# Kernel optimization log

Measured on AMD Instinct MI355X. Metric: run time of the kernel, lower is better.

The kernel has to match this reference:

```python
import jax, jax.numpy as jnp
import numpy as np

L, B, D_IN, D = 96, 32, 4, 128   # leaves, batch, input feats, dim_feedforward
NB, NC = 3, 6                    # n_blocks, n_classes
E = L * (L - 1)                  # directed edges, no self-loops


def _adjacency():
    # one-hot receiver/sender matrices, shape (E, L)
    pairs = np.array([(i, j) for i in range(L) for j in range(L) if i != j])
    recv, send = pairs[:, 0], pairs[:, 1]
    rr = np.zeros((E, L), np.float32); rr[np.arange(E), recv] = 1.0
    rs = np.zeros((E, L), np.float32); rs[np.arange(E), send] = 1.0
    return rr, rs


def setup_inputs() -> dict:
    key = jax.random.key(0)
    ks = jax.random.split(key, 24)
    rr, rs = _adjacency()
    inp = {
        'inputs': jax.random.normal(ks[0], (L, B, D_IN), jnp.float32),
        'rel_rec': jnp.broadcast_to(jnp.asarray(rr), (B, E, L)),
        'rel_send': jnp.broadcast_to(jnp.asarray(rs), (B, E, L)),
    }
    s = 0.1
    # initial MLP: D_IN -> D -> D
    inp['W0a'] = s * jax.random.normal(ks[1], (D_IN, D)); inp['b0a'] = jnp.zeros((D,))
    inp['W0b'] = s * jax.random.normal(ks[2], (D, D));    inp['b0b'] = jnp.zeros((D,))
    # per-block edge MLP (2D -> D -> D) and node MLP (D -> D -> D), stacked over NB
    inp['eW1'] = s * jax.random.normal(ks[3], (NB, 2 * D, D)); inp['eb1'] = jnp.zeros((NB, D))
    inp['eW2'] = s * jax.random.normal(ks[4], (NB, D, D));     inp['eb2'] = jnp.zeros((NB, D))
    inp['nW1'] = s * jax.random.normal(ks[5], (NB, D, D));     inp['nb1'] = jnp.zeros((NB, D))
    inp['nW2'] = s * jax.random.normal(ks[6], (NB, D, D));     inp['nb2'] = jnp.zeros((NB, D))
    # final MLP: 2D -> D -> NC
    inp['fW1'] = s * jax.random.normal(ks[7], (2 * D, D)); inp['fb1'] = jnp.zeros((D,))
    inp['fW2'] = s * jax.random.normal(ks[8], (D, NC));    inp['fb2'] = jnp.zeros((NC,))
    return inp


def _mlp(x, W1, b1, W2, b2):
    return jax.nn.elu(jax.nn.elu(x @ W1 + b1) @ W2 + b2)


def reference(inputs, rel_rec, rel_send, W0a, b0a, W0b, b0b,
              eW1, eb1, eW2, eb2, nW1, nb1, nW2, nb2,
              fW1, fb1, fW2, fb2):
    def node2edge(h):
        # (b,l,d) -> (b,E,2d): cat([senders, receivers])
        senders = jnp.einsum('bel,bld->bed', rel_send, h)
        receivers = jnp.einsum('bel,bld->bed', rel_rec, h)
        return jnp.concatenate([senders, receivers], axis=2)

    def edge2node(h):
        # (b,E,d) -> (b,l,d), mean over incoming edges
        incoming = jnp.einsum('bel,bed->bld', rel_rec, h)
        denom = rel_rec.sum(1)[:, 1]  # (b,)
        return incoming / denom[:, None, None]

    x = jnp.transpose(inputs, (1, 0, 2))           # (b, l, d_in)
    x = _mlp(x, W0a, b0a, W0b, b0b)                # (b, l, D)
    x = node2edge(x)                               # (b, E, 2D)
    for i in range(NB):
        x = _mlp(x, eW1[i], eb1[i], eW2[i], eb2[i])  # (b, E, D)
        x = edge2node(x)                             # (b, l, D)
        x = _mlp(x, nW1[i], nb1[i], nW2[i], nb2[i])  # (b, l, D)
        x = node2edge(x)                             # (b, E, 2D)
    out = jax.nn.elu(x @ fW1 + fb1) @ fW2 + fb2    # (b, E, NC)
    return out
```

## Files before the change

kernel.cpp:

```cpp
#include <hip/hip_runtime.h>
#include <hip/hip_bf16.h>

#define LN 96
#define BN 32
#define DM 128
#define EPN 95

typedef __attribute__((ext_vector_type(8))) short s16x8;
typedef __attribute__((ext_vector_type(4))) float f32x4;

__device__ __forceinline__ float eluf(float x){ return x > 0.f ? x : __expf(x) - 1.f; }
__device__ __forceinline__ unsigned short f2bf(float f){
    unsigned u = __float_as_uint(f);
    return (unsigned short)((u + 0x7fff + ((u >> 16) & 1)) >> 16);
}
__device__ __forceinline__ float bf2f(unsigned short h){ return __uint_as_float(((unsigned)h) << 16); }
__device__ __forceinline__ unsigned cvtpk(float lo, float hi){
    unsigned r;
    asm("v_cvt_pk_bf16_f32 %0, %1, %2" : "=v"(r) : "v"(lo), "v"(hi));
    return r;
}

struct SrcTab { const float* p[19]; };

__global__ void conv_pack_kernel(SrcTab tab, unsigned short* __restrict__ hi,
                                 unsigned short* __restrict__ lo){
    int tid = blockIdx.x * 256 + threadIdx.x;
    int m = tid >> 11, c = tid & 2047;
    int l = c & 63, f = c >> 6;
    int n = (f >> 2) * 16 + (l & 15);
    int k0 = (f & 3) * 32 + (l >> 4) * 8;
    union { unsigned short us[8]; uint4 v; } ph, pl;
#pragma unroll
    for (int e = 0; e < 8; ++e){
        float x;
        if (m == 18) x = (n < 6) ? tab.p[18][(k0 + e) * 6 + n] : 0.f;
        else         x = tab.p[m][(k0 + e) * DM + n];
        unsigned short h = f2bf(x);
        ph.us[e] = h;
        pl.us[e] = f2bf(x - bf2f(h));
    }
    *(uint4*)(hi + (size_t)tid * 8) = ph.v;
    *(uint4*)(lo + (size_t)tid * 8) = pl.v;
}

__device__ __forceinline__ void mmw(const char* atile, int l,
                                    const unsigned short* __restrict__ whW,
                                    const unsigned short* __restrict__ wlW,
                                    f32x4 acc[2]) {
    const int l15 = l & 15, kgrp = l >> 4;
    s16x8 a[4];
#pragma unroll
    for (int ks = 0; ks < 4; ++ks)
        a[ks] = *(const s16x8*)(atile + ((l15 * 256 + (ks * 32 + kgrp * 8) * 2) ^ ((l15 & 7) << 4)));
#pragma unroll
    for (int ntl = 0; ntl < 2; ++ntl) {
#pragma unroll
        for (int ks = 0; ks < 4; ++ks) {
            s16x8 bh = *(const s16x8*)(whW + (size_t)((ntl * 4 + ks) * 64 + l) * 8);
            acc[ntl] = __builtin_amdgcn_mfma_f32_16x16x32_bf16(a[ks], bh, acc[ntl], 0, 0, 0);
        }
#pragma unroll
        for (int ks = 0; ks < 4; ++ks) {
            s16x8 bl = *(const s16x8*)(wlW + (size_t)((ntl * 4 + ks) * 64 + l) * 8);
            acc[ntl] = __builtin_amdgcn_mfma_f32_16x16x32_bf16(a[ks], bl, acc[ntl], 0, 0, 0);
        }
    }
}

__device__ __forceinline__ void store_act(char* atile, int l, int w, f32x4 acc[2]) {
    const int l15 = l & 15, kgrp = l >> 4;
#pragma unroll
    for (int ntl = 0; ntl < 2; ++ntl)
#pragma unroll
        for (int i = 0; i < 4; ++i) {
            int row = kgrp * 4 + i;
            int col = (2 * w + ntl) * 16 + l15;
            *(unsigned short*)(atile + ((row * 256 + col * 2) ^ ((row & 7) << 4))) = f2bf(eluf(acc[ntl][i]));
        }
}

__global__ __launch_bounds__(256) void node0_kernel(
    const float* __restrict__ in,
    const float* __restrict__ W0a, const float* __restrict__ b0a,
    const unsigned short* __restrict__ w2h, const unsigned short* __restrict__ w2l,
    const float* __restrict__ b2,
    const unsigned short* __restrict__ wsh, const unsigned short* __restrict__ wsl,
    const unsigned short* __restrict__ wrh, const unsigned short* __restrict__ wrl,
    const float* __restrict__ bp,
    unsigned short* __restrict__ hs, unsigned short* __restrict__ hr) {
    __shared__ char atile[16 * 256];
    const int t = threadIdx.x;
    const int q = blockIdx.x >> 5, bblk = blockIdx.x & 31;
    const int row0 = bblk * LN + q * 16;
    const int l = t & 63, w = t >> 6;
    const int l15 = l & 15, kgrp = l >> 4;

    {
        int rr = t >> 4, qq = t & 15, c0 = qq * 8;
        int swz = (rr & 7) << 4;
        union { unsigned short us[8]; uint4 v; } pk;
        int row = row0 + rr;
        int b = row / LN, ll = row - b * LN;
        float4 x = *(const float4*)(in + (size_t)(ll * BN + b) * 4);
#pragma unroll
        for (int j = 0; j < 8; ++j) {
            int cc = c0 + j;
            float a = b0a[cc] + x.x * W0a[cc] + x.y * W0a[DM + cc]
                    + x.z * W0a[2 * DM + cc] + x.w * W0a[3 * DM + cc];
            pk.us[j] = f2bf(eluf(a));
        }
        *(uint4*)(atile + ((rr * 256 + c0 * 2) ^ swz)) = pk.v;
    }
    __syncthreads();

    f32x4 acc[2];
    const int cA = (2 * w) * 16 + l15, cB = (2 * w + 1) * 16 + l15;
    {
        float ba = b2[cA], bb = b2[cB];
        acc[0] = (f32x4){ba, ba, ba, ba};
        acc[1] = (f32x4){bb, bb, bb, bb};
        mmw(atile, l, w2h + w * 4096, w2l + w * 4096, acc);
        __syncthreads();
        store_act(atile, l, w, acc);
        __syncthreads();
    }
    acc[0] = (f32x4){0.f, 0.f, 0.f, 0.f};
    acc[1] = (f32x4){0.f, 0.f, 0.f, 0.f};
    mmw(atile, l, wsh + w * 4096, wsl + w * 4096, acc);
#pragma unroll
    for (int ntl = 0; ntl < 2; ++ntl)
#pragma unroll
        for (int i = 0; i < 4; ++i)
            hs[(size_t)(row0 + kgrp * 4 + i) * DM + (2 * w + ntl) * 16 + l15] = f2bf(acc[ntl][i]);
    {
        float ba = bp[cA], bb = bp[cB];
        acc[0] = (f32x4){ba, ba, ba, ba};
        acc[1] = (f32x4){bb, bb, bb, bb};
        mmw(atile, l, wrh + w * 4096, wrl + w * 4096, acc);
    }
#pragma unroll
    for (int ntl = 0; ntl < 2; ++ntl)
#pragma unroll
        for (int i = 0; i < 4; ++i)
            hr[(size_t)(row0 + kgrp * 4 + i) * DM + (2 * w + ntl) * 16 + l15] = f2bf(acc[ntl][i]);
}

__global__ __launch_bounds__(256) void edge_node_kernel(
    const unsigned short* __restrict__ hsIn, const unsigned short* __restrict__ hrIn,
    const unsigned short* __restrict__ whi, const unsigned short* __restrict__ wlo,
    int eslot, const float* __restrict__ eb2v,
    int s1, int s2, int sS,
    const float* __restrict__ b1, const float* __restrict__ b2, const float* __restrict__ bp,
    unsigned short* __restrict__ hsOut, unsigned short* __restrict__ hrOut) {
    __shared__ char tileA[LN * 256];
    __shared__ char tileB[LN * 256];
    __shared__ float hrL[6 * DM];
    __shared__ float gL[6 * DM];
    __shared__ char actA[16 * 256];
    __shared__ char actB[16 * 256];
    const int blk = blockIdx.x;
    const int rg = blk >> 5, b = blk & 31;
    const int r0 = rg * 6;
    const int t = threadIdx.x;
    const int w = t >> 6, l = t & 63;
    const int l15 = l & 15, kgrp = l >> 4;

    if (t < 192) {
        int rr = t >> 5, c4 = (t & 31) * 4;
        ushort4 hv = *(const ushort4*)(hrIn + ((size_t)(b * LN + r0 + rr)) * DM + c4);
        float4 fv = make_float4(bf2f(hv.x), bf2f(hv.y), bf2f(hv.z), bf2f(hv.w));
        *(float4*)(hrL + rr * DM + c4) = fv;
    }
    s16x8 bfr[2][4];
#pragma unroll
    for (int ntl = 0; ntl < 2; ++ntl)
#pragma unroll
        for (int ks = 0; ks < 4; ++ks)
            bfr[ntl][ks] = *(const s16x8*)(whi + (size_t)eslot * 16384 +
                           (size_t)(((2 * w + ntl) * 4 + ks) * 64 + l) * 8);
    float b20 = eb2v[(2 * w) * 16 + l15], b21 = eb2v[(2 * w + 1) * 16 + l15];
    __syncthreads();

    const unsigned short* hsBase = hsIn + (size_t)(b * LN) * DM;
    for (int pr = 0; pr < 3; ++pr) {
        const int rA = r0 + pr * 2, rB = rA + 1;
#pragma unroll
        for (int ch = 0; ch < 6; ++ch) {
            uint4 hv[2];
            int rrs[2], c0s[2], tts[2];
#pragma unroll
            for (int k = 0; k < 2; ++k) {
                int task = t + (ch * 2 + k) * 256;
                int tt = task >= 1536;
                int rem = task - tt * 1536;
                int rr = rem >> 4, c0 = (rem & 15) * 8;
                rrs[k] = rr; c0s[k] = c0; tts[k] = tt;
                int r = tt ? rB : rA;
                int j = rr + (rr >= r);
                hv[k] = *(const uint4*)(hsBase + (size_t)j * DM + c0);
            }
#pragma unroll
            for (int k = 0; k < 2; ++k) {
                int rr = rrs[k], c0 = c0s[k], tt = tts[k];
                const unsigned short* us = (const unsigned short*)&hv[k];
                const float* rp = hrL + (pr * 2 + tt) * DM + c0;
                f32x4 v0 = *(const f32x4*)rp, v1 = *(const f32x4*)(rp + 4);
                float e0 = eluf(bf2f(us[0]) + v0[0]), e1 = eluf(bf2f(us[1]) + v0[1]);
                float e2 = eluf(bf2f(us[2]) + v0[2]), e3 = eluf(bf2f(us[3]) + v0[3]);
                float e4 = eluf(bf2f(us[4]) + v1[0]), e5 = eluf(bf2f(us[5]) + v1[1]);
                float e6 = eluf(bf2f(us[6]) + v1[2]), e7 = eluf(bf2f(us[7]) + v1[3]);
                uint4 pk;
                pk.x = cvtpk(e0, e1); pk.y = cvtpk(e2, e3);
                pk.z = cvtpk(e4, e5); pk.w = cvtpk(e6, e7);
                *(uint4*)((tt ? tileB : tileA) + ((rr * 256 + c0 * 2) ^ ((rr & 7) << 4))) = pk;
            }
        }
        __syncthreads();
#pragma unroll
        for (int slot = 0; slot < 2; ++slot) {
            const char* tile = slot ? tileB : tileA;
            f32x4 acc[6][2] = {};
#pragma unroll
            for (int mt = 0; mt < 6; ++mt) {
                int arow = mt * 16 + l15;
                const char* rb = tile + arow * 256;
                int swz = (arow & 7) << 4;
#pragma unroll
                for (int ks = 0; ks < 4; ++ks) {
                    s16x8 a = *(const s16x8*)(rb + (((ks * 32 + kgrp * 8) * 2) ^ swz));
                    acc[mt][0] = __builtin_amdgcn_mfma_f32_16x16x32_bf16(a, bfr[0][ks], acc[mt][0], 0, 0, 0);
                    acc[mt][1] = __builtin_amdgcn_mfma_f32_16x16x32_bf16(a, bfr[1][ks], acc[mt][1], 0, 0, 0);
                }
            }
            float cs0 = 0.f, cs1 = 0.f;
#pragma unroll
            for (int mt = 0; mt < 6; ++mt)
#pragma unroll
                for (int i = 0; i < 4; ++i) {
                    int row = mt * 16 + kgrp * 4 + i;
                    if (row < EPN) {
                        cs0 += eluf(acc[mt][0][i] + b20);
                        cs1 += eluf(acc[mt][1][i] + b21);
                    }
                }
            cs0 += __shfl_xor(cs0, 16); cs0 += __shfl_xor(cs0, 32);
            cs1 += __shfl_xor(cs1, 16); cs1 += __shfl_xor(cs1, 32);
            if (l < 16) {
                gL[(pr * 2 + slot) * DM + (2 * w) * 16 + l]     = cs0 * (1.f / 95.f);
                gL[(pr * 2 + slot) * DM + (2 * w + 1) * 16 + l] = cs1 * (1.f / 95.f);
            }
        }
        __syncthreads();
    }

    {
        int rr = t >> 4, q = t & 15, c0 = q * 8;
        int swz = (rr & 7) << 4;
        union { unsigned short us[8]; uint4 v; } pk;
        if (rr < 6) {
            const float* src = gL + rr * DM + c0;
            float4 f0 = *(const float4*)(src);
            float4 f1 = *(const float4*)(src + 4);
            pk.us[0] = f2bf(f0.x); pk.us[1] = f2bf(f0.y); pk.us[2] = f2bf(f0.z); pk.us[3] = f2bf(f0.w);
            pk.us[4] = f2bf(f1.x); pk.us[5] = f2bf(f1.y); pk.us[6] = f2bf(f1.z); pk.us[7] = f2bf(f1.w);
        } else pk.v = make_uint4(0, 0, 0, 0);
        *(uint4*)(actA + ((rr * 256 + c0 * 2) ^ swz)) = pk.v;
    }
    __syncthreads();

    f32x4 acc[2];
    const int cA = (2 * w) * 16 + l15, cB = (2 * w + 1) * 16 + l15;
    {
        float ba = b1[cA], bb = b1[cB];
        acc[0] = (f32x4){ba, ba, ba, ba};
        acc[1] = (f32x4){bb, bb, bb, bb};
        mmw(actA, l, whi + (size_t)s1 * 16384 + w * 4096, wlo + (size_t)s1 * 16384 + w * 4096, acc);
        __syncthreads();
        store_act(actB, l, w, acc);
        __syncthreads();
    }
    {
        float ba = b2[cA], bb = b2[cB];
        acc[0] = (f32x4){ba, ba, ba, ba};
        acc[1] = (f32x4){bb, bb, bb, bb};
        mmw(actB, l, whi + (size_t)s2 * 16384 + w * 4096, wlo + (size_t)s2 * 16384 + w * 4096, acc);
        __syncthreads();
        store_act(actA, l, w, acc);
        __syncthreads();
    }
    acc[0] = (f32x4){0.f, 0.f, 0.f, 0.f};
    acc[1] = (f32x4){0.f, 0.f, 0.f, 0.f};
    mmw(actA, l, whi + (size_t)sS * 16384 + w * 4096, wlo + (size_t)sS * 16384 + w * 4096, acc);
#pragma unroll
    for (int ntl = 0; ntl < 2; ++ntl)
#pragma unroll
        for (int i = 0; i < 4; ++i) {
            int row = kgrp * 4 + i;
            if (row < 6)
                hsOut[(size_t)(b * LN + r0 + row) * DM + (2 * w + ntl) * 16 + l15] = f2bf(acc[ntl][i]);
        }
    {
        float ba = bp[cA], bb = bp[cB];
        acc[0] = (f32x4){ba, ba, ba, ba};
        acc[1] = (f32x4){bb, bb, bb, bb};
        mmw(actA, l, whi + (size_t)(sS + 1) * 16384 + w * 4096, wlo + (size_t)(sS + 1) * 16384 + w * 4096, acc);
    }
#pragma unroll
    for (int ntl = 0; ntl < 2; ++ntl)
#pragma unroll
        for (int i = 0; i < 4; ++i) {
            int row = kgrp * 4 + i;
            if (row < 6)
                hrOut[(size_t)(b * LN + r0 + row) * DM + (2 * w + ntl) * 16 + l15] = f2bf(acc[ntl][i]);
        }
}

__global__ __launch_bounds__(256) void final_kernel(
    const unsigned short* __restrict__ hs, const unsigned short* __restrict__ hr,
    const unsigned short* __restrict__ wfh, const unsigned short* __restrict__ wfl,
    const float* __restrict__ fb2, float* __restrict__ out) {
    __shared__ char tA[LN * 256];
    __shared__ char tB[LN * 256];
    __shared__ float hrL[6 * DM];
    const int blk = blockIdx.x;
    const int rg = blk >> 5, b = blk & 31;
    const int r0 = rg * 6;
    const int t = threadIdx.x;
    const int w = t >> 6, l = t & 63;
    const int l15 = l & 15, kgrp = l >> 4;

    if (t < 192) {
        int rr = t >> 5, c4 = (t & 31) * 4;
        ushort4 hv = *(const ushort4*)(hr + ((size_t)(b * LN + r0 + rr)) * DM + c4);
        float4 fv = make_float4(bf2f(hv.x), bf2f(hv.y), bf2f(hv.z), bf2f(hv.w));
        *(float4*)(hrL + rr * DM + c4) = fv;
    }
    s16x8 fh[4], fl4[4];
#pragma unroll
    for (int ks = 0; ks < 4; ++ks) {
        fh[ks]  = *(const s16x8*)(wfh + (size_t)(ks * 64 + l) * 8);
        fl4[ks] = *(const s16x8*)(wfl + (size_t)(ks * 64 + l) * 8);
    }
    float fbv = (l15 < 6) ? fb2[l15] : 0.f;
    __syncthreads();

    const unsigned short* hsBase = hs + (size_t)(b * LN) * DM;
    for (int pr = 0; pr < 3; ++pr) {
        const int rA = r0 + pr * 2, rB = rA + 1;
#pragma unroll
        for (int ch = 0; ch < 6; ++ch) {
            uint4 hv[2];
            int rrs[2], c0s[2], tts[2];
#pragma unroll
            for (int k = 0; k < 2; ++k) {
                int task = t + (ch * 2 + k) * 256;
                int tt = task >= 1536;
                int rem = task - tt * 1536;
                int rr = rem >> 4, c0 = (rem & 15) * 8;
                rrs[k] = rr; c0s[k] = c0; tts[k] = tt;
                int r = tt ? rB : rA;
                int j = rr + (rr >= r);
                hv[k] = *(const uint4*)(hsBase + (size_t)j * DM + c0);
            }
#pragma unroll
            for (int k = 0; k < 2; ++k) {
                int rr = rrs[k], c0 = c0s[k], tt = tts[k];
                const unsigned short* us = (const unsigned short*)&hv[k];
                const float* rp = hrL + (pr * 2 + tt) * DM + c0;
                f32x4 v0 = *(const f32x4*)rp, v1 = *(const f32x4*)(rp + 4);
                float e0 = eluf(bf2f(us[0]) + v0[0]), e1 = eluf(bf2f(us[1]) + v0[1]);
                float e2 = eluf(bf2f(us[2]) + v0[2]), e3 = eluf(bf2f(us[3]) + v0[3]);
                float e4 = eluf(bf2f(us[4]) + v1[0]), e5 = eluf(bf2f(us[5]) + v1[1]);
                float e6 = eluf(bf2f(us[6]) + v1[2]), e7 = eluf(bf2f(us[7]) + v1[3]);
                uint4 pk;
                pk.x = cvtpk(e0, e1); pk.y = cvtpk(e2, e3);
                pk.z = cvtpk(e4, e5); pk.w = cvtpk(e6, e7);
                *(uint4*)((tt ? tB : tA) + ((rr * 256 + c0 * 2) ^ ((rr & 7) << 4))) = pk;
            }
        }
        __syncthreads();
        for (int q = w; q < 12; q += 4) {
            int tt = q >= 6;
            int mt = q - tt * 6;
            const char* tile = tt ? tB : tA;
            int r = tt ? rB : rA;
            int arow = mt * 16 + l15;
            const char* rb = tile + arow * 256;
            int swz = (arow & 7) << 4;
            s16x8 a[4];
#pragma unroll
            for (int ks = 0; ks < 4; ++ks)
                a[ks] = *(const s16x8*)(rb + (((ks * 32 + kgrp * 8) * 2) ^ swz));
            f32x4 acc = (f32x4){fbv, fbv, fbv, fbv};
#pragma unroll
            for (int ks = 0; ks < 4; ++ks)
                acc = __builtin_amdgcn_mfma_f32_16x16x32_bf16(a[ks], fh[ks], acc, 0, 0, 0);
#pragma unroll
            for (int ks = 0; ks < 4; ++ks)
                acc = __builtin_amdgcn_mfma_f32_16x16x32_bf16(a[ks], fl4[ks], acc, 0, 0, 0);
            if (l15 < 6) {
                float* ob = out + ((size_t)b * (LN * EPN) + (size_t)r * EPN) * 6;
#pragma unroll
                for (int i = 0; i < 4; ++i) {
                    int row = mt * 16 + kgrp * 4 + i;
                    if (row < EPN) ob[(size_t)row * 6 + l15] = acc[i];
                }
            }
        }
        __syncthreads();
    }
}

extern "C" void kernel_launch(void* const* d_in, const int* in_sizes, int n_in,
                              void* d_out, int out_size, void* d_ws, size_t ws_size,
                              hipStream_t stream) {
    const float* inputs = (const float*)d_in[0];
    const float* W0a = (const float*)d_in[3];
    const float* b0a = (const float*)d_in[4];
    const float* W0b = (const float*)d_in[5];
    const float* b0b = (const float*)d_in[6];
    const float* eW1 = (const float*)d_in[7];
    const float* eb1 = (const float*)d_in[8];
    const float* eW2 = (const float*)d_in[9];
    const float* eb2 = (const float*)d_in[10];
    const float* nW1 = (const float*)d_in[11];
    const float* nb1 = (const float*)d_in[12];
    const float* nW2 = (const float*)d_in[13];
    const float* nb2 = (const float*)d_in[14];
    const float* fW1 = (const float*)d_in[15];
    const float* fb1 = (const float*)d_in[16];
    const float* fW2 = (const float*)d_in[17];
    const float* fb2 = (const float*)d_in[18];
    float* out = (float*)d_out;

    const int NR = BN * LN;
    unsigned short* whi = (unsigned short*)d_ws;
    unsigned short* wlo = whi + 19 * 16384;
    unsigned short* hsA = wlo + 19 * 16384;
    unsigned short* hrA = hsA + (NR + 1) * DM;
    unsigned short* hsB = hrA + NR * DM;
    unsigned short* hrB = hsB + (NR + 1) * DM;

    SrcTab tab;
    tab.p[0] = eW2;          tab.p[1] = eW2 + 16384;  tab.p[2] = eW2 + 32768;
    tab.p[3] = W0b;
    tab.p[4] = eW1;          tab.p[5] = eW1 + 16384;
    tab.p[6] = nW1;          tab.p[7] = nW2;          tab.p[8] = eW1 + 32768;  tab.p[9]  = eW1 + 49152;
    tab.p[10] = nW1 + 16384; tab.p[11] = nW2 + 16384; tab.p[12] = eW1 + 65536; tab.p[13] = eW1 + 81920;
    tab.p[14] = nW1 + 32768; tab.p[15] = nW2 + 32768; tab.p[16] = fW1;         tab.p[17] = fW1 + 16384;
    tab.p[18] = fW2;

    #define WM(m) (whi + (m) * 16384), (wlo + (m) * 16384)

    conv_pack_kernel<<<152, 256, 0, stream>>>(tab, whi, wlo);
    node0_kernel<<<192, 256, 0, stream>>>(inputs, W0a, b0a, WM(3), b0b, WM(4), WM(5), eb1, hsA, hrA);
    edge_node_kernel<<<512, 256, 0, stream>>>(hsA, hrA, whi, wlo, 0, eb2,
                                              6, 7, 8, nb1, nb2, eb1 + DM, hsB, hrB);
    edge_node_kernel<<<512, 256, 0, stream>>>(hsB, hrB, whi, wlo, 1, eb2 + DM,
                                              10, 11, 12, nb1 + DM, nb2 + DM, eb1 + 2 * DM, hsA, hrA);
    edge_node_kernel<<<512, 256, 0, stream>>>(hsA, hrA, whi, wlo, 2, eb2 + 2 * DM,
                                              14, 15, 16, nb1 + 2 * DM, nb2 + 2 * DM, fb1, hsB, hrB);
    final_kernel<<<512, 256, 0, stream>>>(hsB, hrB, WM(18), fb2, out);
    #undef WM
}
```

Measured before the change: 118.3 us.

## Split edge_node work into 4-node groups and alias shared memory buffers

Each edge_node block now handles 4 receiver nodes instead of 6, raising the grid from 512 to 768 blocks so the work spreads more evenly across CUs. The shared-memory buffers are merged into one aliased region, with the small activation tiles reusing the edge tile space and hrL/gL stored as bf16, which shrinks LDS per block and may allow more resident blocks. The cost is more blocks each reloading the edge weights and repeating the small node MLP, plus slightly lower precision on the cached hr values.

Result: slower. 122.2 us (+3.4%).

```diff
diff --git a/kernel.cpp b/kernel.cpp
--- a/kernel.cpp
+++ b/kernel.cpp
@@ -153,24 +153,23 @@
     int s1, int s2, int sS,
     const float* __restrict__ b1, const float* __restrict__ b2, const float* __restrict__ bp,
     unsigned short* __restrict__ hsOut, unsigned short* __restrict__ hrOut) {
-    __shared__ char tileA[LN * 256];
-    __shared__ char tileB[LN * 256];
-    __shared__ float hrL[6 * DM];
-    __shared__ float gL[6 * DM];
-    __shared__ char actA[16 * 256];
-    __shared__ char actB[16 * 256];
+    __shared__ char smem[49152 + 1024 + 1024];
+    char* tileA = smem;
+    char* tileB = smem + 24576;
+    unsigned short* hrL = (unsigned short*)(smem + 49152);
+    unsigned short* gL  = (unsigned short*)(smem + 49152 + 1024);
+    char* actA = smem;
+    char* actB = smem + 4096;
     const int blk = blockIdx.x;
     const int rg = blk >> 5, b = blk & 31;
-    const int r0 = rg * 6;
+    const int r0 = rg * 4;
     const int t = threadIdx.x;
     const int w = t >> 6, l = t & 63;
     const int l15 = l & 15, kgrp = l >> 4;
 
-    if (t < 192) {
-        int rr = t >> 5, c4 = (t & 31) * 4;
-        ushort4 hv = *(const ushort4*)(hrIn + ((size_t)(b * LN + r0 + rr)) * DM + c4);
-        float4 fv = make_float4(bf2f(hv.x), bf2f(hv.y), bf2f(hv.z), bf2f(hv.w));
-        *(float4*)(hrL + rr * DM + c4) = fv;
+    if (t < 64) {
+        int rr = t >> 4, c8 = (t & 15) * 8;
+        *(uint4*)(hrL + rr * DM + c8) = *(const uint4*)(hrIn + ((size_t)(b * LN + r0 + rr)) * DM + c8);
     }
     s16x8 bfr[2][4];
 #pragma unroll
@@ -183,7 +182,7 @@
     __syncthreads();
 
     const unsigned short* hsBase = hsIn + (size_t)(b * LN) * DM;
-    for (int pr = 0; pr < 3; ++pr) {
+    for (int pr = 0; pr < 2; ++pr) {
         const int rA = r0 + pr * 2, rB = rA + 1;
 #pragma unroll
         for (int ch = 0; ch < 6; ++ch) {
@@ -204,12 +203,12 @@
             for (int k = 0; k < 2; ++k) {
                 int rr = rrs[k], c0 = c0s[k], tt = tts[k];
                 const unsigned short* us = (const unsigned short*)&hv[k];
-                const float* rp = hrL + (pr * 2 + tt) * DM + c0;
-                f32x4 v0 = *(const f32x4*)rp, v1 = *(const f32x4*)(rp + 4);
-                float e0 = eluf(bf2f(us[0]) + v0[0]), e1 = eluf(bf2f(us[1]) + v0[1]);
-                float e2 = eluf(bf2f(us[2]) + v0[2]), e3 = eluf(bf2f(us[3]) + v0[3]);
-                float e4 = eluf(bf2f(us[4]) + v1[0]), e5 = eluf(bf2f(us[5]) + v1[1]);
-                float e6 = eluf(bf2f(us[6]) + v1[2]), e7 = eluf(bf2f(us[7]) + v1[3]);
+                uint4 rv = *(const uint4*)(hrL + (pr * 2 + tt) * DM + c0);
+                const unsigned short* ur = (const unsigned short*)&rv;
+                float e0 = eluf(bf2f(us[0]) + bf2f(ur[0])), e1 = eluf(bf2f(us[1]) + bf2f(ur[1]));
+                float e2 = eluf(bf2f(us[2]) + bf2f(ur[2])), e3 = eluf(bf2f(us[3]) + bf2f(ur[3]));
+                float e4 = eluf(bf2f(us[4]) + bf2f(ur[4])), e5 = eluf(bf2f(us[5]) + bf2f(ur[5]));
+                float e6 = eluf(bf2f(us[6]) + bf2f(ur[6])), e7 = eluf(bf2f(us[7]) + bf2f(ur[7]));
                 uint4 pk;
                 pk.x = cvtpk(e0, e1); pk.y = cvtpk(e2, e3);
                 pk.z = cvtpk(e4, e5); pk.w = cvtpk(e6, e7);
@@ -247,8 +246,8 @@
             cs0 += __shfl_xor(cs0, 16); cs0 += __shfl_xor(cs0, 32);
             cs1 += __shfl_xor(cs1, 16); cs1 += __shfl_xor(cs1, 32);
             if (l < 16) {
-                gL[(pr * 2 + slot) * DM + (2 * w) * 16 + l]     = cs0 * (1.f / 95.f);
-                gL[(pr * 2 + slot) * DM + (2 * w + 1) * 16 + l] = cs1 * (1.f / 95.f);
+                gL[(pr * 2 + slot) * DM + (2 * w) * 16 + l]     = f2bf(cs0 * (1.f / 95.f));
+                gL[(pr * 2 + slot) * DM + (2 * w + 1) * 16 + l] = f2bf(cs1 * (1.f / 95.f));
             }
         }
         __syncthreads();
@@ -257,15 +256,10 @@
     {
         int rr = t >> 4, q = t & 15, c0 = q * 8;
         int swz = (rr & 7) << 4;
-        union { unsigned short us[8]; uint4 v; } pk;
-        if (rr < 6) {
-            const float* src = gL + rr * DM + c0;
-            float4 f0 = *(const float4*)(src);
-            float4 f1 = *(const float4*)(src + 4);
-            pk.us[0] = f2bf(f0.x); pk.us[1] = f2bf(f0.y); pk.us[2] = f2bf(f0.z); pk.us[3] = f2bf(f0.w);
-            pk.us[4] = f2bf(f1.x); pk.us[5] = f2bf(f1.y); pk.us[6] = f2bf(f1.z); pk.us[7] = f2bf(f1.w);
-        } else pk.v = make_uint4(0, 0, 0, 0);
-        *(uint4*)(actA + ((rr * 256 + c0 * 2) ^ swz)) = pk.v;
+        uint4 pk;
+        if (rr < 4) pk = *(const uint4*)(gL + rr * DM + c0);
+        else        pk = make_uint4(0, 0, 0, 0);
+        *(uint4*)(actA + ((rr * 256 + c0 * 2) ^ swz)) = pk;
     }
     __syncthreads();
 
@@ -297,7 +291,7 @@
 #pragma unroll
         for (int i = 0; i < 4; ++i) {
             int row = kgrp * 4 + i;
-            if (row < 6)
+            if (row < 4)
                 hsOut[(size_t)(b * LN + r0 + row) * DM + (2 * w + ntl) * 16 + l15] = f2bf(acc[ntl][i]);
         }
     {
@@ -311,7 +305,7 @@
 #pragma unroll
         for (int i = 0; i < 4; ++i) {
             int row = kgrp * 4 + i;
-            if (row < 6)
+            if (row < 4)
                 hrOut[(size_t)(b * LN + r0 + row) * DM + (2 * w + ntl) * 16 + l15] = f2bf(acc[ntl][i]);
         }
 }
@@ -455,11 +449,11 @@
 
     conv_pack_kernel<<<152, 256, 0, stream>>>(tab, whi, wlo);
     node0_kernel<<<192, 256, 0, stream>>>(inputs, W0a, b0a, WM(3), b0b, WM(4), WM(5), eb1, hsA, hrA);
-    edge_node_kernel<<<512, 256, 0, stream>>>(hsA, hrA, whi, wlo, 0, eb2,
+    edge_node_kernel<<<768, 256, 0, stream>>>(hsA, hrA, whi, wlo, 0, eb2,
                                               6, 7, 8, nb1, nb2, eb1 + DM, hsB, hrB);
-    edge_node_kernel<<<512, 256, 0, stream>>>(hsB, hrB, whi, wlo, 1, eb2 + DM,
+    edge_node_kernel<<<768, 256, 0, stream>>>(hsB, hrB, whi, wlo, 1, eb2 + DM,
                                               10, 11, 12, nb1 + DM, nb2 + DM, eb1 + 2 * DM, hsA, hrA);
-    edge_node_kernel<<<512, 256, 0, stream>>>(hsA, hrA, whi, wlo, 2, eb2 + 2 * DM,
+    edge_node_kernel<<<768, 256, 0, stream>>>(hsA, hrA, whi, wlo, 2, eb2 + 2 * DM,
                                               14, 15, 16, nb1 + 2 * DM, nb2 + 2 * DM, fb1, hsB, hrB);
     final_kernel<<<512, 256, 0, stream>>>(hsB, hrB, WM(18), fb2, out);
     #undef WM
```
